# Kernel tuning notes

Measured on AMD Instinct MI355X. Metric: run time of the kernel, lower is better.

Reference implementation:

```python
import jax, jax.numpy as jnp
import numpy as np

FORGET_BIAS = 1.0

def _lstm_cell(x, h, c, W, b):
    # BasicLSTMCell: z = [x, h] @ W + b, gates in (i, j, f, o) order
    z = jnp.concatenate([x, h], axis=-1) @ W + b
    i, j, f, o = jnp.split(z, 4, axis=-1)
    c_new = c * jax.nn.sigmoid(f + FORGET_BIAS) + jax.nn.sigmoid(i) * jnp.tanh(j)
    h_new = jnp.tanh(c_new) * jax.nn.sigmoid(o)
    return h_new, c_new

def setup_inputs() -> dict:
    key = jax.random.key(0)
    k1, k2, k3, k4, k5, k6 = jax.random.split(key, 6)
    B, T, D = 256, 200, 512
    rnn_input = jax.random.normal(k1, (B, T, D), dtype=jnp.float32)
    seq_len = jax.random.randint(k2, (B,), 0, T, dtype=jnp.int32)
    s = 0.05
    W0 = jax.random.normal(k3, (2 * D, 4 * D), dtype=jnp.float32) * s
    b0 = jax.random.normal(k4, (4 * D,), dtype=jnp.float32) * s
    W1 = jax.random.normal(k5, (2 * D, 4 * D), dtype=jnp.float32) * s
    b1 = jax.random.normal(k6, (4 * D,), dtype=jnp.float32) * s
    return {"rnn_input": rnn_input, "seq_len": seq_len, "W0": W0, "b0": b0, "W1": W1, "b1": b1}

def reference(rnn_input, seq_len, W0, b0, W1, b1):
    B, T, D = rnn_input.shape
    h0 = jnp.zeros((B, D), rnn_input.dtype)
    init = (h0, h0, h0, h0)  # (h_l0, c_l0, h_l1, c_l1)

    def step(carry, inp):
        h0, c0, h1, c1 = carry
        x_t, t = inp
        # layer 0 (plain LSTM)
        h0n, c0n = _lstm_cell(x_t, h0, c0, W0, b0)
        # layer 1 (ResidualWrapper: out = cell_out + input)
        h1n, c1n = _lstm_cell(h0n, h1, c1, W1, b1)
        y = h1n + h0n
        # dynamic_rnn semantics: past seq_len, output zero and state copy-through
        valid = (t < seq_len)[:, None]
        h0n = jnp.where(valid, h0n, h0)
        c0n = jnp.where(valid, c0n, c0)
        h1n = jnp.where(valid, h1n, h1)
        c1n = jnp.where(valid, c1n, c1)
        y = jnp.where(valid, y, 0.0)
        return (h0n, c0n, h1n, c1n), y

    xs = (jnp.swapaxes(rnn_input, 0, 1), jnp.arange(T, dtype=seq_len.dtype))
    _, ys = jax.lax.scan(step, init, xs)  # ys: [T, B, D]
    return jnp.swapaxes(ys, 0, 1)  # [B, T, D]
```

## Files before the change

kernel.cpp:

```cpp
#include <hip/hip_runtime.h>

using short8 = __attribute__((ext_vector_type(8))) short;
using f32x4  = __attribute__((ext_vector_type(4))) float;
typedef unsigned short u16;
typedef unsigned int   u32;
typedef unsigned long long u64;

constexpr int Bn = 256;
constexpr int Tn = 200;
constexpr int Dn = 512;

__device__ __forceinline__ u16 f2bf(float x) {
  union { float f; unsigned u; } v; v.f = x;
  unsigned r = v.u + 0x7FFFu + ((v.u >> 16) & 1u);
  return (u16)(r >> 16);
}
__device__ __forceinline__ float sigm(float x) { return 1.0f / (1.0f + __expf(-x)); }
__device__ __forceinline__ float tanhe(float x) { return 1.0f - 2.0f / (__expf(2.0f * x) + 1.0f); }

__global__ void cvt_x_frag(const float* __restrict__ x, u16* __restrict__ xf) {
  int i = blockIdx.x * 256 + threadIdx.x;
  int lane = i & 63;
  int kkd  = (i >> 6) & 15;
  int rf   = (i >> 10) & 3;
  int mt_t = i >> 12;
  int t = mt_t % 200, mtile = mt_t / 200;
  int row = mtile * 64 + rf * 16 + (lane & 15);
  int k0  = kkd * 32 + (lane >> 4) * 8;
  const float* s = x + ((size_t)row * Tn + t) * Dn + k0;
  float4 v0 = *reinterpret_cast<const float4*>(s);
  float4 v1 = *reinterpret_cast<const float4*>(s + 4);
  short8 r;
  r[0]=(short)f2bf(v0.x); r[1]=(short)f2bf(v0.y); r[2]=(short)f2bf(v0.z); r[3]=(short)f2bf(v0.w);
  r[4]=(short)f2bf(v1.x); r[5]=(short)f2bf(v1.y); r[6]=(short)f2bf(v1.z); r[7]=(short)f2bf(v1.w);
  reinterpret_cast<short8*>(xf)[i] = r;
}

__global__ void cvt_w_frag(const float* __restrict__ W0, const float* __restrict__ W1,
                           u16* __restrict__ Wf) {
  __shared__ u16 T[64][65];
  int b = blockIdx.x;
  int nt = b & 31, kt = (b >> 5) & 15, role = b >> 9;
  const float* W = role ? W1 : W0;
  int t = threadIdx.x;
  int k0 = kt * 64, n0 = nt * 64;
  int kr = t >> 6, nl = t & 63;
#pragma unroll
  for (int r = 0; r < 16; ++r) {
    int k = r * 4 + kr;
    T[k][nl] = f2bf(W[(size_t)(k0 + k) * 2048 + n0 + nl]);
  }
  __syncthreads();
  int g = n0 >> 9;
  int dslBase = (n0 & 511) >> 4;
  int kkBase  = k0 >> 5;
  int lane = t & 63, grp = t >> 6;
  int lr = lane & 15, lk = lane >> 4;
#pragma unroll
  for (int c = grp; c < 8; c += 4) {
    int dslL = c & 3, kkL = c >> 2;
    int dsl = dslBase + dslL, kk = kkBase + kkL;
    short8 v;
#pragma unroll
    for (int e = 0; e < 8; ++e)
      v[e] = (short)T[kkL * 32 + lk * 8 + e][dslL * 16 + lr];
    *reinterpret_cast<short8*>(Wf + ((((size_t)(role * 32 + dsl) * 4 + g) * 32 + kk) * 64 + lane) * 8) = v;
  }
}

#define MFMA16 __builtin_amdgcn_mfma_f32_16x16x32_bf16
#define GLOAD_LDS(g, l) __builtin_amdgcn_global_load_lds(                    \
    (const __attribute__((address_space(1))) void*)(g),                      \
    (__attribute__((address_space(3))) void*)(l), 16, 0, 0)

#define ISS4C(A0, A1, A2, A3, P)                                             \
  asm volatile("global_load_dwordx4 %0, %4, off sc0 sc1\n\t"                 \
               "global_load_dwordx4 %1, %4, off offset:1024 sc0 sc1\n\t"     \
               "global_load_dwordx4 %2, %4, off offset:2048 sc0 sc1\n\t"     \
               "global_load_dwordx4 %3, %4, off offset:3072 sc0 sc1"         \
               : "=v"(A0), "=v"(A1), "=v"(A2), "=v"(A3) : "v"(P))
#define ISS4L(A0, A1, A2, A3, P)                                             \
  asm volatile("global_load_dwordx4 %0, %4, off sc0\n\t"                     \
               "global_load_dwordx4 %1, %4, off offset:1024 sc0\n\t"         \
               "global_load_dwordx4 %2, %4, off offset:2048 sc0\n\t"         \
               "global_load_dwordx4 %3, %4, off offset:3072 sc0"             \
               : "=v"(A0), "=v"(A1), "=v"(A2), "=v"(A3) : "v"(P))
#define ISS4N(A0, A1, A2, A3, P)                                             \
  asm volatile("global_load_dwordx4 %0, %4, off\n\t"                         \
               "global_load_dwordx4 %1, %4, off offset:1024\n\t"             \
               "global_load_dwordx4 %2, %4, off offset:2048\n\t"             \
               "global_load_dwordx4 %3, %4, off offset:3072"                 \
               : "=v"(A0), "=v"(A1), "=v"(A2), "=v"(A3) : "v"(P))
#define WAITV(N)                                                             \
  asm volatile("s_waitcnt vmcnt(" #N ")" ::: "memory");                      \
  __builtin_amdgcn_sched_barrier(0)
#define MMK(av, kk) {                                                        \
    short8 w0 = *reinterpret_cast<const short8*>(WL + (kk) * 1024);          \
    short8 w1 = *reinterpret_cast<const short8*>(WL + 32768 + (kk) * 1024);  \
    short8 w2 = *reinterpret_cast<const short8*>(WL + 65536 + (kk) * 1024);  \
    short8 w3 = *reinterpret_cast<const short8*>(WL + 98304 + (kk) * 1024);  \
    ac0 = MFMA16(av, w0, ac0, 0, 0, 0);                                      \
    ac1 = MFMA16(av, w1, ac1, 0, 0, 0);                                      \
    ac2 = MFMA16(av, w2, ac2, 0, 0, 0);                                      \
    ac3 = MFMA16(av, w3, ac3, 0, 0, 0); }

extern "C" __global__ void __launch_bounds__(256, 1)
rnn_persist(const u16* __restrict__ xf, const u16* __restrict__ Wf,
            const float* __restrict__ b0, const float* __restrict__ b1,
            const int* __restrict__ seq,
            u16* __restrict__ hf0, u16* __restrict__ hf1, u16* __restrict__ hx,
            u32* __restrict__ bar, float* __restrict__ out) {
  extern __shared__ __align__(16) char smem[];
  const int blk = blockIdx.x;
  const int q = blk & 7;
  const int role = q & 1;
  const int mtile = q >> 1;
  const int dsl = blk >> 3;
  const int tid = threadIdx.x;
  const int rf = tid >> 6, lane = tid & 63;

  {
    const char* gsrc = reinterpret_cast<const char*>(Wf)
                     + (size_t)(role * 32 + dsl) * 131072 + tid * 16;
    char* lds = smem + tid * 16;
#pragma unroll
    for (int i = 0; i < 32; ++i)
      GLOAD_LDS(gsrc + i * 4096, lds + i * 4096);
  }

  const char* xfb = reinterpret_cast<const char*>(xf);
  const char* h0b = reinterpret_cast<const char*>(hf0);
  const char* h1b = reinterpret_cast<const char*>(hf1);
  const char* hxb = reinterpret_cast<const char*>(hx);
  const int aoff = rf * 16384 + lane * 16;
  const char* WL = smem + lane * 16;

  const int d0 = dsl * 16 + (lane & 15);
  const float* bias = role ? b1 : b0;
  const float bg0 = bias[d0], bg1 = bias[512 + d0], bg2 = bias[1024 + d0], bg3 = bias[1536 + d0];
  const int rowB = mtile * 64 + rf * 16 + (lane >> 4) * 4;
  int sl[4];
#pragma unroll
  for (int e = 0; e < 4; ++e) sl[e] = seq[rowB + e];

  const int kkd = dsl >> 1;
  const int lane_t_base = ((((dsl & 1) << 1) | ((lane & 15) >> 3)) << 4) + (lane >> 4) * 4;
  const size_t hoff0 = (size_t)mtile * 32768 + (size_t)(rf * 16 + kkd) * 512
                     + (size_t)lane_t_base * 8 + (lane & 7);

  u16* hfSelf = role ? hf1 : hf0;
  u16* stg = reinterpret_cast<u16*>(smem + 131072);
  const size_t o8 = (size_t)((mtile * 4 + rf) * 16 + kkd) * 128
                  + ((dsl & 1) * 32 + (lane >> 1)) * 2 + (lane & 1);
  u32* flagme = bar + mtile * 64 + role * 32 + dsl;
  const u32* fb = bar + mtile * 64 + tid;

  float creg[4]  = {0.f, 0.f, 0.f, 0.f};
  float hkeep[4] = {0.f, 0.f, 0.f, 0.f};

  __syncthreads();

#pragma unroll 1
  for (int p = 0; p <= Tn; ++p) {
    const bool act = role ? (p >= 1) : (p < Tn);
    const int Rp = (p & 1) ^ 1, Wp = p & 1;
    if (act) {
      const int tcur = role ? (p - 1) : p;
      const size_t hRp = (size_t)Rp * 262144 + (size_t)mtile * 65536;

      short8 A0,A1,A2,A3,A4,A5,A6,A7,A8,A9,A10,A11,A12,A13,A14,A15;
      short8 B0,B1,B2,B3,B4,B5,B6,B7,B8,B9,B10,B11,B12,B13,B14,B15;
      u32 hn0, hn1, hn2, hn3;

      {
        const char* Bh = (role == 0) ? h0b + hRp + aoff : h1b + hRp + aoff;
        ISS4L(B0,B1,B2,B3,    Bh);
        ISS4L(B4,B5,B6,B7,    Bh + 4096);
        ISS4L(B8,B9,B10,B11,  Bh + 8192);
        ISS4L(B12,B13,B14,B15,Bh + 12288);
      }
      if (role) {
        const char* hra = hxb + (size_t)Rp * 262144 + hoff0 * 2;
        asm volatile("global_load_ushort %0, %4, off sc0 sc1\n\t"
                     "global_load_ushort %1, %4, off offset:16 sc0 sc1\n\t"
                     "global_load_ushort %2, %4, off offset:32 sc0 sc1\n\t"
                     "global_load_ushort %3, %4, off offset:48 sc0 sc1"
                     : "=v"(hn0), "=v"(hn1), "=v"(hn2), "=v"(hn3) : "v"(hra));
      } else {
        const char* hra = h0b + (size_t)Rp * 262144 + hoff0 * 2;
        asm volatile("global_load_ushort %0, %4, off sc0\n\t"
                     "global_load_ushort %1, %4, off offset:16 sc0\n\t"
                     "global_load_ushort %2, %4, off offset:32 sc0\n\t"
                     "global_load_ushort %3, %4, off offset:48 sc0"
                     : "=v"(hn0), "=v"(hn1), "=v"(hn2), "=v"(hn3) : "v"(hra));
      }
      if (role == 0) {
        const char* Alo = xfb + ((size_t)mtile * Tn + p) * 65536 + aoff;
        ISS4N(A0,A1,A2,A3,    Alo);
        ISS4N(A4,A5,A6,A7,    Alo + 4096);
        ISS4N(A8,A9,A10,A11,  Alo + 8192);
        ISS4N(A12,A13,A14,A15,Alo + 12288);
      } else {
        const char* Alo = hxb + hRp + aoff;
        ISS4C(A0,A1,A2,A3,    Alo);
        ISS4C(A4,A5,A6,A7,    Alo + 4096);
        ISS4C(A8,A9,A10,A11,  Alo + 8192);
        ISS4C(A12,A13,A14,A15,Alo + 12288);
      }

      f32x4 ac0 = {0.f,0.f,0.f,0.f}, ac1 = {0.f,0.f,0.f,0.f};
      f32x4 ac2 = {0.f,0.f,0.f,0.f}, ac3 = {0.f,0.f,0.f,0.f};

      WAITV(32); MMK(B0,16) MMK(B1,17) MMK(B2,18) MMK(B3,19)
      WAITV(28); MMK(B4,20) MMK(B5,21) MMK(B6,22) MMK(B7,23)
      WAITV(24); MMK(B8,24) MMK(B9,25) MMK(B10,26) MMK(B11,27)
      WAITV(20); MMK(B12,28) MMK(B13,29) MMK(B14,30) MMK(B15,31)
      WAITV(12); MMK(A0,0)  MMK(A1,1)  MMK(A2,2)  MMK(A3,3)
      WAITV(8);  MMK(A4,4)  MMK(A5,5)  MMK(A6,6)  MMK(A7,7)
      WAITV(4);  MMK(A8,8)  MMK(A9,9)  MMK(A10,10) MMK(A11,11)
      WAITV(0);  MMK(A12,12) MMK(A13,13) MMK(A14,14) MMK(A15,15)

      const u32 hnv[4] = {hn0, hn1, hn2, hn3};
#pragma unroll
      for (int e = 0; e < 4; ++e) {
        float zi = ac0[e] + bg0, zj = ac1[e] + bg1, zf = ac2[e] + bg2, zo = ac3[e] + bg3;
        float cprev = creg[e];
        float cn = cprev * sigm(zf + 1.0f) + sigm(zi) * tanhe(zj);
        float hn = tanhe(cn) * sigm(zo);
        bool valid = tcur < sl[e];
        float hk = valid ? hn : hkeep[e];
        creg[e] = valid ? cn : cprev;
        hkeep[e] = hk;
        stg[rf * 256 + (((lane & 15) >> 3) * 16 + (lane >> 4) * 4 + e) * 8 + (lane & 7)] = f2bf(hk);
        if (role) {
          union { float f; u32 u; } hv; hv.u = hnv[e] << 16;
          out[((size_t)(rowB + e) * Tn + tcur) * Dn + d0] = valid ? (hn + hv.f) : 0.0f;
        }
      }
      __syncthreads();
      {
        u64 v = reinterpret_cast<const u64*>(stg)[tid];
        u64* ha = reinterpret_cast<u64*>(hfSelf + (size_t)Wp * 131072) + o8;
        asm volatile("global_store_dwordx2 %0, %1, off sc0" :: "v"(ha), "v"(v) : "memory");
        if (role == 0) {
          u64* he = reinterpret_cast<u64*>(hx + (size_t)Wp * 131072) + o8;
          asm volatile("global_store_dwordx2 %0, %1, off sc0 sc1" :: "v"(he), "v"(v) : "memory");
        }
      }
      asm volatile("s_waitcnt vmcnt(0)" ::: "memory");
    }

    if (p == Tn) break;

    __syncthreads();
    if (tid == 0) {
      u32 tv = (u32)(p + 1);
      asm volatile("global_store_dword %0, %1, off sc0 sc1" :: "v"(flagme), "v"(tv) : "memory");
    }
    if (tid < 64) {
      const int tgt = p + 1;
      u32 fv;
      do {
        asm volatile("global_load_dword %0, %1, off sc0 sc1\n\t"
                     "s_waitcnt vmcnt(0)"
                     : "=v"(fv) : "v"(fb) : "memory");
      } while (!__all((int)fv >= tgt));
    }
    __syncthreads();
  }
}

#define LDA(kk) (*reinterpret_cast<const short8*>(                           \
    (kk) < 16 ? (Alo + (size_t)(kk) * 1024) : (Ahi + (size_t)((kk) - 16) * 1024)))

extern "C" __global__ void __launch_bounds__(256, 1)
rnn_step(const u16* __restrict__ xf, const u16* __restrict__ Wf,
         const float* __restrict__ b0, const float* __restrict__ b1,
         const int* __restrict__ seq,
         u16* __restrict__ hf0, u16* __restrict__ hf1,
         float* __restrict__ cbuf, float* __restrict__ out, int p) {
  extern __shared__ __align__(16) char smem[];
  const int blk = blockIdx.x;
  const int role = blk & 1;
  const int mtile = (blk >> 1) & 3;
  const int dsl = blk >> 3;
  const bool act = role ? (p >= 1) : (p < Tn);
  if (!act) return;

  const int tid = threadIdx.x;
  const int rf = tid >> 6, lane = tid & 63;
  const int Rp = (p & 1) ^ 1, Wp = p & 1;
  const int tcur = role ? (p - 1) : p;

  {
    const char* gsrc = reinterpret_cast<const char*>(Wf)
                     + (size_t)(role * 32 + dsl) * 131072 + tid * 16;
    char* lds = smem + tid * 16;
#pragma unroll
    for (int i = 0; i < 32; ++i)
      GLOAD_LDS(gsrc + i * 4096, lds + i * 4096);
  }

  const char* h0base = reinterpret_cast<const char*>(hf0);
  const char* h1base = reinterpret_cast<const char*>(hf1);
  const size_t hRp = (size_t)Rp * 262144 + (size_t)mtile * 65536;
  const int aoff = rf * 16384 + lane * 16;

  const char* Alo;
  const char* Ahi;
  if (role == 0) {
    Alo = reinterpret_cast<const char*>(xf) + ((size_t)mtile * Tn + p) * 65536 + aoff;
    Ahi = h0base + hRp + aoff;
  } else {
    Alo = h0base + hRp + aoff;
    Ahi = h1base + hRp + aoff;
  }
  const char* WL = smem + lane * 16;

  short8 ca0 = LDA(0), ca1 = LDA(1), ca2 = LDA(2), ca3 = LDA(3);

  const int d0 = dsl * 16 + (lane & 15);
  const float* bias = role ? b1 : b0;
  const float bg0 = bias[d0], bg1 = bias[512 + d0], bg2 = bias[1024 + d0], bg3 = bias[1536 + d0];
  const int rowB = mtile * 64 + rf * 16 + (lane >> 4) * 4;
  int sl[4];
#pragma unroll
  for (int e = 0; e < 4; ++e) sl[e] = seq[rowB + e];

  const int kkd = dsl >> 1;
  const int lane_t_base = ((((dsl & 1) << 1) | ((lane & 15) >> 3)) << 4) + (lane >> 4) * 4;
  const size_t hoff0 = (size_t)mtile * 32768 + (size_t)(rf * 16 + kkd) * 512
                     + (size_t)lane_t_base * 8 + (lane & 7);

  u16 h0nraw[4];
  if (role) {
    const u16* hr = reinterpret_cast<const u16*>(h0base) + (size_t)Rp * 131072;
#pragma unroll
    for (int e = 0; e < 4; ++e) h0nraw[e] = hr[hoff0 + e * 8];
  }
  float* cme = cbuf + ((size_t)blk * 256 + tid) * 4;
  float cpre[4];
#pragma unroll
  for (int e = 0; e < 4; ++e) cpre[e] = cme[e];
  u16* hfSelf = role ? hf1 : hf0;
  const u16* hprev = hfSelf + (size_t)Rp * 131072;
  u16 hp16[4];
#pragma unroll
  for (int e = 0; e < 4; ++e) hp16[e] = hprev[hoff0 + e * 8];

  __syncthreads();

  f32x4 ac0 = {0.f,0.f,0.f,0.f}, ac1 = {0.f,0.f,0.f,0.f};
  f32x4 ac2 = {0.f,0.f,0.f,0.f}, ac3 = {0.f,0.f,0.f,0.f};
  short8 na0, na1, na2, na3;
#pragma unroll
  for (int c = 0; c < 8; ++c) {
    const int k0 = c * 4;
    if (c < 7) {
      na0 = LDA(k0 + 4); na1 = LDA(k0 + 5); na2 = LDA(k0 + 6); na3 = LDA(k0 + 7);
    }
#pragma unroll
    for (int j = 0; j < 4; ++j) {
      const int kk = k0 + j;
      short8 a = (j == 0) ? ca0 : (j == 1) ? ca1 : (j == 2) ? ca2 : ca3;
      short8 w0 = *reinterpret_cast<const short8*>(WL + kk * 1024);
      short8 w1 = *reinterpret_cast<const short8*>(WL + 32768 + kk * 1024);
      short8 w2 = *reinterpret_cast<const short8*>(WL + 65536 + kk * 1024);
      short8 w3 = *reinterpret_cast<const short8*>(WL + 98304 + kk * 1024);
      ac0 = MFMA16(a, w0, ac0, 0, 0, 0);
      ac1 = MFMA16(a, w1, ac1, 0, 0, 0);
      ac2 = MFMA16(a, w2, ac2, 0, 0, 0);
      ac3 = MFMA16(a, w3, ac3, 0, 0, 0);
    }
    ca0 = na0; ca1 = na1; ca2 = na2; ca3 = na3;
  }

  u16* stg = reinterpret_cast<u16*>(smem + 131072);
#pragma unroll
  for (int e = 0; e < 4; ++e) {
    float zi = ac0[e] + bg0, zj = ac1[e] + bg1, zf = ac2[e] + bg2, zo = ac3[e] + bg3;
    float cprev = cpre[e];
    float cn = cprev * sigm(zf + 1.0f) + sigm(zi) * tanhe(zj);
    float hn = tanhe(cn) * sigm(zo);
    bool valid = tcur < sl[e];
    union { float f; u32 u; } hp; hp.u = ((u32)hp16[e]) << 16;
    float hkeep = valid ? hn : hp.f;
    cme[e] = valid ? cn : cprev;
    stg[rf * 256 + (((lane & 15) >> 3) * 16 + (lane >> 4) * 4 + e) * 8 + (lane & 7)] = f2bf(hkeep);
    if (role) {
      union { float f; u32 u; } hv; hv.u = ((u32)h0nraw[e]) << 16;
      out[((size_t)(rowB + e) * Tn + tcur) * Dn + d0] = valid ? (hn + hv.f) : 0.0f;
    }
  }
  __syncthreads();
  {
    const int rft = tid >> 6, u = tid & 63;
    u64 v = reinterpret_cast<const u64*>(stg)[tid];
    u64* hw8 = reinterpret_cast<u64*>(hfSelf + (size_t)Wp * 131072);
    size_t o8 = (size_t)((mtile * 4 + rft) * 16 + kkd) * 128 + ((dsl & 1) * 32 + (u >> 1)) * 2 + (u & 1);
    hw8[o8] = v;
  }
}

extern "C" void kernel_launch(void* const* d_in, const int* in_sizes, int n_in,
                              void* d_out, int out_size, void* d_ws, size_t ws_size,
                              hipStream_t stream) {
  (void)in_sizes; (void)n_in; (void)out_size; (void)ws_size;
  const float* x  = (const float*)d_in[0];
  const int* seq  = (const int*)d_in[1];
  const float* W0 = (const float*)d_in[2];
  const float* b0 = (const float*)d_in[3];
  const float* W1 = (const float*)d_in[4];
  const float* b1 = (const float*)d_in[5];
  float* out = (float*)d_out;

  char* ws = (char*)d_ws;
  u16*  xf   = (u16*)(ws);
  u16*  Wf   = (u16*)(ws + 52428800);
  u16*  hf0  = (u16*)(ws + 60817408);
  u16*  hf1  = (u16*)(ws + 61341696);
  u32*  bar  = (u32*)(ws + 61865984);
  u16*  hx   = (u16*)(ws + 61870080);
  float* cbuf = (float*)(ws + 61865984);

  hipMemsetAsync(ws + 60817408, 0, 2097152, stream);
  hipLaunchKernelGGL(cvt_x_frag, dim3(12800), dim3(256), 0, stream, x, xf);
  hipLaunchKernelGGL(cvt_w_frag, dim3(1024), dim3(256), 0, stream, W0, W1, Wf);

  hipFuncSetAttribute((const void*)rnn_persist,
                      hipFuncAttributeMaxDynamicSharedMemorySize, 133120);
  hipFuncSetAttribute((const void*)rnn_step,
                      hipFuncAttributeMaxDynamicSharedMemorySize, 133120);

  void* args[] = { (void*)&xf, (void*)&Wf, (void*)&b0, (void*)&b1, (void*)&seq,
                   (void*)&hf0, (void*)&hf1, (void*)&hx, (void*)&bar, (void*)&out };
  hipError_t err = hipLaunchCooperativeKernel((void*)rnn_persist, dim3(256), dim3(256),
                                              args, 133120, stream);
  if (err != hipSuccess) {
    for (int p = 0; p <= Tn; ++p) {
      hipLaunchKernelGGL(rnn_step, dim3(256), dim3(256), 133120, stream,
                         xf, Wf, b0, b1, seq, hf0, hf1, cbuf, out, p);
    }
  }
}
```

Baseline: 1.133 ms.

## Split K across wave pairs with two row tiles per wave and LDS reduction

Each block's four waves used to cover one 16-row slice each across the full K of 32 chunks. Now they form pairs that split K in half, each wave covering two row slices, so every weight fragment read from LDS feeds two MFMAs. Partial sums are exchanged through a new LDS region, and a block barrier sits before the gate math. The aim is to halve LDS weight traffic per MFMA, at the cost of more accumulator registers, an extra barrier and 16KB more shared memory.

After: 1.114 ms (median of 2 runs). No clear change (-1.6%).

```diff
diff --git a/kernel.cpp b/kernel.cpp
--- a/kernel.cpp
+++ b/kernel.cpp
@@ -94,15 +94,15 @@
 #define WAITV(N)                                                             \
   asm volatile("s_waitcnt vmcnt(" #N ")" ::: "memory");                      \
   __builtin_amdgcn_sched_barrier(0)
-#define MMK(av, kk) {                                                        \
-    short8 w0 = *reinterpret_cast<const short8*>(WL + (kk) * 1024);          \
-    short8 w1 = *reinterpret_cast<const short8*>(WL + 32768 + (kk) * 1024);  \
-    short8 w2 = *reinterpret_cast<const short8*>(WL + 65536 + (kk) * 1024);  \
-    short8 w3 = *reinterpret_cast<const short8*>(WL + 98304 + (kk) * 1024);  \
-    ac0 = MFMA16(av, w0, ac0, 0, 0, 0);                                      \
-    ac1 = MFMA16(av, w1, ac1, 0, 0, 0);                                      \
-    ac2 = MFMA16(av, w2, ac2, 0, 0, 0);                                      \
-    ac3 = MFMA16(av, w3, ac3, 0, 0, 0); }
+#define MMK2(alo, ahi, kki) {                                                \
+    short8 w0 = *reinterpret_cast<const short8*>(WK + (kki) * 1024);         \
+    short8 w1 = *reinterpret_cast<const short8*>(WK + 32768 + (kki) * 1024); \
+    short8 w2 = *reinterpret_cast<const short8*>(WK + 65536 + (kki) * 1024); \
+    short8 w3 = *reinterpret_cast<const short8*>(WK + 98304 + (kki) * 1024); \
+    pa0 = MFMA16(alo, w0, pa0, 0, 0, 0); qa0 = MFMA16(ahi, w0, qa0, 0, 0, 0);\
+    pa1 = MFMA16(alo, w1, pa1, 0, 0, 0); qa1 = MFMA16(ahi, w1, qa1, 0, 0, 0);\
+    pa2 = MFMA16(alo, w2, pa2, 0, 0, 0); qa2 = MFMA16(ahi, w2, qa2, 0, 0, 0);\
+    pa3 = MFMA16(alo, w3, pa3, 0, 0, 0); qa3 = MFMA16(ahi, w3, qa3, 0, 0, 0); }
 
 extern "C" __global__ void __launch_bounds__(256, 1)
 rnn_persist(const u16* __restrict__ xf, const u16* __restrict__ Wf,
@@ -117,7 +117,11 @@
   const int mtile = q >> 1;
   const int dsl = blk >> 3;
   const int tid = threadIdx.x;
-  const int rf = tid >> 6, lane = tid & 63;
+  const int wid = tid >> 6, lane = tid & 63;
+  const int rr = wid & 1, ks = wid >> 1;
+  const int rLo = rr * 2;
+  const int rF  = rr * 2 + ks;
+  const int rO  = rr * 2 + (1 - ks);
 
   {
     const char* gsrc = reinterpret_cast<const char*>(Wf)
@@ -132,28 +136,31 @@
   const char* h0b = reinterpret_cast<const char*>(hf0);
   const char* h1b = reinterpret_cast<const char*>(hf1);
   const char* hxb = reinterpret_cast<const char*>(hx);
-  const int aoff = rf * 16384 + lane * 16;
-  const char* WL = smem + lane * 16;
+  const char* WK = smem + lane * 16 + ks * 16384;
+  f32x4* redv = reinterpret_cast<f32x4*>(smem + 131072);
+  u16* stg = reinterpret_cast<u16*>(smem + 147456);
 
   const int d0 = dsl * 16 + (lane & 15);
   const float* bias = role ? b1 : b0;
   const float bg0 = bias[d0], bg1 = bias[512 + d0], bg2 = bias[1024 + d0], bg3 = bias[1536 + d0];
-  const int rowB = mtile * 64 + rf * 16 + (lane >> 4) * 4;
+  const int rowB = mtile * 64 + rF * 16 + (lane >> 4) * 4;
   int sl[4];
 #pragma unroll
   for (int e = 0; e < 4; ++e) sl[e] = seq[rowB + e];
 
   const int kkd = dsl >> 1;
   const int lane_t_base = ((((dsl & 1) << 1) | ((lane & 15) >> 3)) << 4) + (lane >> 4) * 4;
-  const size_t hoff0 = (size_t)mtile * 32768 + (size_t)(rf * 16 + kkd) * 512
+  const size_t hoff0 = (size_t)mtile * 32768 + (size_t)(rF * 16 + kkd) * 512
                      + (size_t)lane_t_base * 8 + (lane & 7);
 
   u16* hfSelf = role ? hf1 : hf0;
-  u16* stg = reinterpret_cast<u16*>(smem + 131072);
-  const size_t o8 = (size_t)((mtile * 4 + rf) * 16 + kkd) * 128
+  const size_t o8 = (size_t)((mtile * 4 + rF) * 16 + kkd) * 128
                   + ((dsl & 1) * 32 + (lane >> 1)) * 2 + (lane & 1);
   u32* flagme = bar + mtile * 64 + role * 32 + dsl;
   const u32* fb = bar + mtile * 64 + tid;
+
+  const int aoffLo = rLo * 16384 + lane * 16;
+  const int aoffHi = aoffLo + 16384;
 
   float creg[4]  = {0.f, 0.f, 0.f, 0.f};
   float hkeep[4] = {0.f, 0.f, 0.f, 0.f};
@@ -172,13 +179,6 @@
       short8 B0,B1,B2,B3,B4,B5,B6,B7,B8,B9,B10,B11,B12,B13,B14,B15;
       u32 hn0, hn1, hn2, hn3;
 
-      {
-        const char* Bh = (role == 0) ? h0b + hRp + aoff : h1b + hRp + aoff;
-        ISS4L(B0,B1,B2,B3,    Bh);
-        ISS4L(B4,B5,B6,B7,    Bh + 4096);
-        ISS4L(B8,B9,B10,B11,  Bh + 8192);
-        ISS4L(B12,B13,B14,B15,Bh + 12288);
-      }
       if (role) {
         const char* hra = hxb + (size_t)Rp * 262144 + hoff0 * 2;
         asm volatile("global_load_ushort %0, %4, off sc0 sc1\n\t"
@@ -194,31 +194,65 @@
                      "global_load_ushort %3, %4, off offset:48 sc0"
                      : "=v"(hn0), "=v"(hn1), "=v"(hn2), "=v"(hn3) : "v"(hra));
       }
-      if (role == 0) {
-        const char* Alo = xfb + ((size_t)mtile * Tn + p) * 65536 + aoff;
-        ISS4N(A0,A1,A2,A3,    Alo);
-        ISS4N(A4,A5,A6,A7,    Alo + 4096);
-        ISS4N(A8,A9,A10,A11,  Alo + 8192);
-        ISS4N(A12,A13,A14,A15,Alo + 12288);
+      if (role == 0 && ks == 0) {
+        const char* base = xfb + ((size_t)mtile * Tn + p) * 65536;
+        const char* Lb = base + aoffLo; const char* Hb = base + aoffHi;
+        ISS4N(A0,A1,A2,A3,    Lb);          ISS4N(B0,B1,B2,B3,    Hb);
+        ISS4N(A4,A5,A6,A7,    Lb + 4096);   ISS4N(B4,B5,B6,B7,    Hb + 4096);
+        ISS4N(A8,A9,A10,A11,  Lb + 8192);   ISS4N(B8,B9,B10,B11,  Hb + 8192);
+        ISS4N(A12,A13,A14,A15,Lb + 12288);  ISS4N(B12,B13,B14,B15,Hb + 12288);
+      } else if (role == 0) {
+        const char* base = h0b + hRp;
+        const char* Lb = base + aoffLo; const char* Hb = base + aoffHi;
+        ISS4L(A0,A1,A2,A3,    Lb);          ISS4L(B0,B1,B2,B3,    Hb);
+        ISS4L(A4,A5,A6,A7,    Lb + 4096);   ISS4L(B4,B5,B6,B7,    Hb + 4096);
+        ISS4L(A8,A9,A10,A11,  Lb + 8192);   ISS4L(B8,B9,B10,B11,  Hb + 8192);
+        ISS4L(A12,A13,A14,A15,Lb + 12288);  ISS4L(B12,B13,B14,B15,Hb + 12288);
+      } else if (ks == 0) {
+        const char* base = hxb + hRp;
+        const char* Lb = base + aoffLo; const char* Hb = base + aoffHi;
+        ISS4C(A0,A1,A2,A3,    Lb);          ISS4C(B0,B1,B2,B3,    Hb);
+        ISS4C(A4,A5,A6,A7,    Lb + 4096);   ISS4C(B4,B5,B6,B7,    Hb + 4096);
+        ISS4C(A8,A9,A10,A11,  Lb + 8192);   ISS4C(B8,B9,B10,B11,  Hb + 8192);
+        ISS4C(A12,A13,A14,A15,Lb + 12288);  ISS4C(B12,B13,B14,B15,Hb + 12288);
       } else {
-        const char* Alo = hxb + hRp + aoff;
-        ISS4C(A0,A1,A2,A3,    Alo);
-        ISS4C(A4,A5,A6,A7,    Alo + 4096);
-        ISS4C(A8,A9,A10,A11,  Alo + 8192);
-        ISS4C(A12,A13,A14,A15,Alo + 12288);
+        const char* base = h1b + hRp;
+        const char* Lb = base + aoffLo; const char* Hb = base + aoffHi;
+        ISS4L(A0,A1,A2,A3,    Lb);          ISS4L(B0,B1,B2,B3,    Hb);
+        ISS4L(A4,A5,A6,A7,    Lb + 4096);   ISS4L(B4,B5,B6,B7,    Hb + 4096);
+        ISS4L(A8,A9,A10,A11,  Lb + 8192);   ISS4L(B8,B9,B10,B11,  Hb + 8192);
+        ISS4L(A12,A13,A14,A15,Lb + 12288);  ISS4L(B12,B13,B14,B15,Hb + 12288);
       }
 
-      f32x4 ac0 = {0.f,0.f,0.f,0.f}, ac1 = {0.f,0.f,0.f,0.f};
-      f32x4 ac2 = {0.f,0.f,0.f,0.f}, ac3 = {0.f,0.f,0.f,0.f};
-
-      WAITV(32); MMK(B0,16) MMK(B1,17) MMK(B2,18) MMK(B3,19)
-      WAITV(28); MMK(B4,20) MMK(B5,21) MMK(B6,22) MMK(B7,23)
-      WAITV(24); MMK(B8,24) MMK(B9,25) MMK(B10,26) MMK(B11,27)
-      WAITV(20); MMK(B12,28) MMK(B13,29) MMK(B14,30) MMK(B15,31)
-      WAITV(12); MMK(A0,0)  MMK(A1,1)  MMK(A2,2)  MMK(A3,3)
-      WAITV(8);  MMK(A4,4)  MMK(A5,5)  MMK(A6,6)  MMK(A7,7)
-      WAITV(4);  MMK(A8,8)  MMK(A9,9)  MMK(A10,10) MMK(A11,11)
-      WAITV(0);  MMK(A12,12) MMK(A13,13) MMK(A14,14) MMK(A15,15)
+      f32x4 pa0 = {0.f,0.f,0.f,0.f}, pa1 = {0.f,0.f,0.f,0.f};
+      f32x4 pa2 = {0.f,0.f,0.f,0.f}, pa3 = {0.f,0.f,0.f,0.f};
+      f32x4 qa0 = {0.f,0.f,0.f,0.f}, qa1 = {0.f,0.f,0.f,0.f};
+      f32x4 qa2 = {0.f,0.f,0.f,0.f}, qa3 = {0.f,0.f,0.f,0.f};
+
+      WAITV(24); MMK2(A0,B0,0)   MMK2(A1,B1,1)   MMK2(A2,B2,2)   MMK2(A3,B3,3)
+      WAITV(16); MMK2(A4,B4,4)   MMK2(A5,B5,5)   MMK2(A6,B6,6)   MMK2(A7,B7,7)
+      WAITV(8);  MMK2(A8,B8,8)   MMK2(A9,B9,9)   MMK2(A10,B10,10) MMK2(A11,B11,11)
+      WAITV(0);  MMK2(A12,B12,12) MMK2(A13,B13,13) MMK2(A14,B14,14) MMK2(A15,B15,15)
+
+      {
+        f32x4 s0 = (ks == 0) ? qa0 : pa0;
+        f32x4 s1 = (ks == 0) ? qa1 : pa1;
+        f32x4 s2 = (ks == 0) ? qa2 : pa2;
+        f32x4 s3 = (ks == 0) ? qa3 : pa3;
+        redv[(rO * 4 + 0) * 64 + lane] = s0;
+        redv[(rO * 4 + 1) * 64 + lane] = s1;
+        redv[(rO * 4 + 2) * 64 + lane] = s2;
+        redv[(rO * 4 + 3) * 64 + lane] = s3;
+      }
+      __syncthreads();
+      f32x4 ac0 = (ks == 0) ? pa0 : qa0;
+      f32x4 ac1 = (ks == 0) ? pa1 : qa1;
+      f32x4 ac2 = (ks == 0) ? pa2 : qa2;
+      f32x4 ac3 = (ks == 0) ? pa3 : qa3;
+      ac0 += redv[(rF * 4 + 0) * 64 + lane];
+      ac1 += redv[(rF * 4 + 1) * 64 + lane];
+      ac2 += redv[(rF * 4 + 2) * 64 + lane];
+      ac3 += redv[(rF * 4 + 3) * 64 + lane];
 
       const u32 hnv[4] = {hn0, hn1, hn2, hn3};
 #pragma unroll
@@ -231,15 +265,15 @@
         float hk = valid ? hn : hkeep[e];
         creg[e] = valid ? cn : cprev;
         hkeep[e] = hk;
-        stg[rf * 256 + (((lane & 15) >> 3) * 16 + (lane >> 4) * 4 + e) * 8 + (lane & 7)] = f2bf(hk);
+        stg[rF * 256 + (((lane & 15) >> 3) * 16 + (lane >> 4) * 4 + e) * 8 + (lane & 7)] = f2bf(hk);
         if (role) {
           union { float f; u32 u; } hv; hv.u = hnv[e] << 16;
           out[((size_t)(rowB + e) * Tn + tcur) * Dn + d0] = valid ? (hn + hv.f) : 0.0f;
         }
       }
-      __syncthreads();
+      asm volatile("s_waitcnt lgkmcnt(0)" ::: "memory");
       {
-        u64 v = reinterpret_cast<const u64*>(stg)[tid];
+        u64 v = reinterpret_cast<const u64*>(stg)[rF * 64 + lane];
         u64* ha = reinterpret_cast<u64*>(hfSelf + (size_t)Wp * 131072) + o8;
         asm volatile("global_store_dwordx2 %0, %1, off sc0" :: "v"(ha), "v"(v) : "memory");
         if (role == 0) {
@@ -270,6 +304,15 @@
   }
 }
 
+#define MMK(av, kk) {                                                        \
+    short8 w0 = *reinterpret_cast<const short8*>(WL + (kk) * 1024);          \
+    short8 w1 = *reinterpret_cast<const short8*>(WL + 32768 + (kk) * 1024);  \
+    short8 w2 = *reinterpret_cast<const short8*>(WL + 65536 + (kk) * 1024);  \
+    short8 w3 = *reinterpret_cast<const short8*>(WL + 98304 + (kk) * 1024);  \
+    ac0 = MFMA16(av, w0, ac0, 0, 0, 0);                                      \
+    ac1 = MFMA16(av, w1, ac1, 0, 0, 0);                                      \
+    ac2 = MFMA16(av, w2, ac2, 0, 0, 0);                                      \
+    ac3 = MFMA16(av, w3, ac3, 0, 0, 0); }
 #define LDA(kk) (*reinterpret_cast<const short8*>(                           \
     (kk) < 16 ? (Alo + (size_t)(kk) * 1024) : (Ahi + (size_t)((kk) - 16) * 1024)))
 
@@ -363,14 +406,7 @@
     for (int j = 0; j < 4; ++j) {
       const int kk = k0 + j;
       short8 a = (j == 0) ? ca0 : (j == 1) ? ca1 : (j == 2) ? ca2 : ca3;
-      short8 w0 = *reinterpret_cast<const short8*>(WL + kk * 1024);
-      short8 w1 = *reinterpret_cast<const short8*>(WL + 32768 + kk * 1024);
-      short8 w2 = *reinterpret_cast<const short8*>(WL + 65536 + kk * 1024);
-      short8 w3 = *reinterpret_cast<const short8*>(WL + 98304 + kk * 1024);
-      ac0 = MFMA16(a, w0, ac0, 0, 0, 0);
-      ac1 = MFMA16(a, w1, ac1, 0, 0, 0);
-      ac2 = MFMA16(a, w2, ac2, 0, 0, 0);
-      ac3 = MFMA16(a, w3, ac3, 0, 0, 0);
+      MMK(a, kk)
     }
     ca0 = na0; ca1 = na1; ca2 = na2; ca3 = na3;
   }
@@ -428,14 +464,14 @@
   hipLaunchKernelGGL(cvt_w_frag, dim3(1024), dim3(256), 0, stream, W0, W1, Wf);
 
   hipFuncSetAttribute((const void*)rnn_persist,
-                      hipFuncAttributeMaxDynamicSharedMemorySize, 133120);
+                      hipFuncAttributeMaxDynamicSharedMemorySize, 149504);
   hipFuncSetAttribute((const void*)rnn_step,
                       hipFuncAttributeMaxDynamicSharedMemorySize, 133120);
 
   void* args[] = { (void*)&xf, (void*)&Wf, (void*)&b0, (void*)&b1, (void*)&seq,
                    (void*)&hf0, (void*)&hf1, (void*)&hx, (void*)&bar, (void*)&out };
   hipError_t err = hipLaunchCooperativeKernel((void*)rnn_persist, dim3(256), dim3(256),
-                                              args, 133120, stream);
+                                              args, 149504, stream);
   if (err != hipSuccess) {
     for (int p = 0; p <= Tn; ++p) {
       hipLaunchKernelGGL(rnn_step, dim3(256), dim3(256), 133120, stream,
```
